# Optimization experiments

Hardware: AMD Instinct MI355X
Metric: run time of the kernel (lower is better)

## Reference

```python
import jax, jax.numpy as jnp
import numpy as np
import math

D_PAIR = 64
N_HEADS = 4
D_HEAD = D_PAIR // N_HEADS


def setup_inputs() -> dict:
    key = jax.random.key(0)
    ks = jax.random.split(key, 9)
    B, L, D = 2, 256, D_PAIR
    s = 1.0 / math.sqrt(D)
    return {
        "z": jax.random.normal(ks[0], (B, L, L, D), dtype=jnp.float32),
        "ln_scale": jnp.ones((D,), jnp.float32),
        "ln_bias": jnp.zeros((D,), jnp.float32),
        "Wq": jax.random.normal(ks[1], (D, D), jnp.float32) * s,
        "Wk": jax.random.normal(ks[2], (D, D), jnp.float32) * s,
        "Wv": jax.random.normal(ks[3], (D, D), jnp.float32) * s,
        "Wg": jax.random.normal(ks[4], (D, D), jnp.float32) * s,
        "bg": jax.random.normal(ks[5], (D,), jnp.float32) * 0.02,
        "Wo": jax.random.normal(ks[6], (D, D), jnp.float32) * s,
        "bo": jax.random.normal(ks[7], (D,), jnp.float32) * 0.02,
    }


def _layernorm(x, scale, bias, eps=1e-5):
    mu = jnp.mean(x, axis=-1, keepdims=True)
    var = jnp.var(x, axis=-1, keepdims=True)
    return (x - mu) * jax.lax.rsqrt(var + eps) * scale + bias


def reference(z, ln_scale, ln_bias, Wq, Wk, Wv, Wg, bg, Wo, bo):
    B, L, _, D = z.shape
    H, Dh = N_HEADS, D_HEAD
    zn = _layernorm(z, ln_scale, ln_bias)
    # torch Linear(no bias): x @ W.T
    Q = (zn @ Wq.T).reshape(B, L, L, H, Dh)
    K = (zn @ Wk.T).reshape(B, L, L, H, Dh)
    V = (zn @ Wv.T).reshape(B, L, L, H, Dh)
    scale = 1.0 / math.sqrt(Dh)
    # row-wise attention: for each row l, attend over column index j
    attn = jnp.einsum("blihd,bljhd->blhij", Q, K) * scale  # [B,L,H,L,L]
    attn = jax.nn.softmax(attn, axis=-1)
    out = jnp.einsum("blhij,bljhd->blihd", attn, V).reshape(B, L, L, D)
    gate = jax.nn.sigmoid(zn @ Wg.T + bg)
    out = gate * out
    return out @ Wo.T + bo
```

## Files before the change

kernel.cpp:

```cpp
#include <hip/hip_runtime.h>
#include <hip/hip_bf16.h>
#include <math.h>


typedef __attribute__((ext_vector_type(4))) float f32x4;
typedef __attribute__((ext_vector_type(8))) short s16x8;

#define MFMA16(a, b, c) __builtin_amdgcn_mfma_f32_16x16x32_bf16((a), (b), (c), 0, 0, 0)

__device__ __forceinline__ unsigned pk2(float a, float b) {
    union { __hip_bfloat162 h; unsigned u; } c;
    float2 t; t.x = a; t.y = b;
    c.h = __float22bfloat162_rn(t);
    return c.u;
}
__device__ __forceinline__ s16x8 cvt8(const float* p) {
    union { unsigned u[4]; s16x8 v; } r;
    r.u[0] = pk2(p[0], p[1]); r.u[1] = pk2(p[2], p[3]);
    r.u[2] = pk2(p[4], p[5]); r.u[3] = pk2(p[6], p[7]);
    return r.v;
}

static constexpr int ZNL = 0;
static constexpr int KSH = 16384;
static constexpr int VT  = 20480;
static constexpr int LDS_EL = 24704;

__global__ __launch_bounds__(256, 3)
void ka_fused(const float* __restrict__ z, const float* __restrict__ ln_s,
              const float* __restrict__ ln_b, const float* __restrict__ Wq,
              const float* __restrict__ Wk, const float* __restrict__ Wv,
              const float* __restrict__ Wg, const float* __restrict__ bg,
              short* __restrict__ ws)
{
    __shared__ __align__(16) short lds[LDS_EL];
    const int tid = threadIdx.x, lane = tid & 63, w = tid >> 6;
    const int n16 = lane & 15, quad = lane >> 4;
    const bool qlo = (quad < 2);
    const int g = blockIdx.x, bl = g >> 2, h = g & 3;
    const size_t rowbase = (size_t)bl * (256 * 64);
    const int wsl = w * 4096;

    {
        float zn[64];
        const float4* zp4 = (const float4*)(z + rowbase + (size_t)tid * 64);
        #pragma unroll
        for (int gq = 0; gq < 16; ++gq) {
            float4 v4 = zp4[gq];
            zn[gq * 4 + 0] = v4.x; zn[gq * 4 + 1] = v4.y;
            zn[gq * 4 + 2] = v4.z; zn[gq * 4 + 3] = v4.w;
        }
        float mu = 0.f;
        #pragma unroll
        for (int k = 0; k < 64; ++k) mu += zn[k];
        mu *= (1.f / 64.f);
        float va = 0.f;
        #pragma unroll
        for (int k = 0; k < 64; ++k) { float d = zn[k] - mu; va += d * d; }
        const float rs = rsqrtf(va * (1.f / 64.f) + 1e-5f);
        #pragma unroll
        for (int k = 0; k < 64; ++k) zn[k] = (zn[k] - mu) * rs * ln_s[k] + ln_b[k];
        const int lr = lane;
        #pragma unroll
        for (int gq = 0; gq < 8; ++gq) {
            union { unsigned u[4]; s16x8 v; } pkv;
            pkv.u[0] = pk2(zn[gq * 8 + 0], zn[gq * 8 + 1]);
            pkv.u[1] = pk2(zn[gq * 8 + 2], zn[gq * 8 + 3]);
            pkv.u[2] = pk2(zn[gq * 8 + 4], zn[gq * 8 + 5]);
            pkv.u[3] = pk2(zn[gq * 8 + 6], zn[gq * 8 + 7]);
            *(s16x8*)&lds[ZNL + wsl + (lr >> 4) * 1024 + (lr & 15) * 64
                          + ((gq ^ (lr & 7)) * 8)] = pkv.v;
        }
    }

    s16x8 bq[2], bk[2], bv[2], bgf[2];
    #pragma unroll
    for (int ks = 0; ks < 2; ++ks) {
        size_t off = (size_t)(h * 16 + n16) * 64 + ks * 32 + quad * 8;
        bq[ks] = cvt8(Wq + off);  bk[ks] = cvt8(Wk + off);
        bv[ks] = cvt8(Wv + off);  bgf[ks] = cvt8(Wg + off);
    }
    const float4 bg4 = *(const float4*)(bg + h * 16 + quad * 4);
    constexpr float QS = 0.25f * 1.44269504088896340736f;

    float g4t[4][4];
    #pragma unroll
    for (int t = 0; t < 4; ++t) {
        s16x8 zn0 = *(const s16x8*)&lds[ZNL + wsl + t * 1024 + n16 * 64
                                        + ((quad ^ (n16 & 7)) * 8)];
        s16x8 zn1 = *(const s16x8*)&lds[ZNL + wsl + t * 1024 + n16 * 64
                                        + (((4 + quad) ^ (n16 & 7)) * 8)];
        f32x4 aq = {}, ak = {}, av = {}, ag = {};
        aq = MFMA16(bq[0], zn0, aq);  aq = MFMA16(bq[1], zn1, aq);
        ak = MFMA16(bk[0], zn0, ak);  ak = MFMA16(bk[1], zn1, ak);
        ag = MFMA16(bgf[0], zn0, ag); ag = MFMA16(bgf[1], zn1, ag);
        av = MFMA16(zn0, bv[0], av);  av = MFMA16(zn1, bv[1], av);
        {
            uint2 p = {pk2(aq[0] * QS, aq[1] * QS), pk2(aq[2] * QS, aq[3] * QS)};
            *(uint2*)&lds[ZNL + wsl + t * 1024 + n16 * 16 + quad * 4] = p;
        }
        {
            uint2 p = {pk2(ak[0], ak[1]), pk2(ak[2], ak[3])};
            *(uint2*)&lds[KSH + (w * 64 + t * 16 + n16) * 16 + quad * 4] = p;
        }
        {
            uint2 p = {pk2(av[0], av[1]), pk2(av[2], av[3])};
            *(uint2*)&lds[VT + n16 * 264 + (w * 64 + t * 16 + quad * 4)] = p;
        }
        #pragma unroll
        for (int r = 0; r < 4; ++r)
            g4t[t][r] = 1.f / (1.f + __expf(-(ag[r] + bg4[r])));
    }

    s16x8 qa[4];
    #pragma unroll
    for (int qt = 0; qt < 4; ++qt) {
        s16x8 q = {};
        if (qlo) q = *(const s16x8*)&lds[ZNL + wsl + qt * 1024 + n16 * 16 + quad * 8];
        qa[qt] = q;
    }
    __syncthreads();

    float lrow[4][4];
    f32x4 o4[4];
    #pragma unroll
    for (int qt = 0; qt < 4; ++qt) {
        o4[qt] = {};
        #pragma unroll
        for (int r = 0; r < 4; ++r) lrow[qt][r] = 0.f;
    }
    const int sw = (n16 ^ (n16 >> 2)) & 3;
    for (int ch = 0; ch < 8; ++ch) {
        #pragma unroll
        for (int jtl = 0; jtl < 2; ++jtl) {
            int jt = ch * 2 + jtl;
            s16x8 kf = {};
            if (qlo) kf = *(const s16x8*)&lds[KSH + (jt * 16 + n16) * 16 + quad * 8];
            const int po = (((jtl * 2 + (quad >> 1)) ^ sw) * 8) + (quad & 1) * 4;
            #pragma unroll
            for (int qt = 0; qt < 4; ++qt) {
                f32x4 zc = {};
                f32x4 s = MFMA16(kf, qa[qt], zc);
                float e0 = exp2f(s[0]), e1 = exp2f(s[1]);
                float e2 = exp2f(s[2]), e3 = exp2f(s[3]);
                lrow[qt][0] += e0; lrow[qt][1] += e1;
                lrow[qt][2] += e2; lrow[qt][3] += e3;
                uint2 p = {pk2(e0, e1), pk2(e2, e3)};
                *(uint2*)&lds[ZNL + wsl + qt * 1024 + 256 + n16 * 40 + po] = p;
            }
        }
        s16x8 vf = *(const s16x8*)&lds[VT + n16 * 264 + ch * 32 + quad * 8];
        #pragma unroll
        for (int qt = 0; qt < 4; ++qt) {
            s16x8 pf = *(const s16x8*)&lds[ZNL + wsl + qt * 1024 + 256 + n16 * 40
                                           + ((quad ^ sw) * 8)];
            o4[qt] = MFMA16(vf, pf, o4[qt]);
        }
    }

    #pragma unroll
    for (int qt = 0; qt < 4; ++qt) {
        float l = lrow[qt][0] + lrow[qt][1] + lrow[qt][2] + lrow[qt][3];
        l += __shfl_xor(l, 16);
        l += __shfl_xor(l, 32);
        const float inv = 1.f / l;
        float g0 = g4t[qt][0] * o4[qt][0] * inv;
        float g1 = g4t[qt][1] * o4[qt][1] * inv;
        float g2 = g4t[qt][2] * o4[qt][2] * inv;
        float g3 = g4t[qt][3] * o4[qt][3] * inv;
        uint2 p = {pk2(g0, g1), pk2(g2, g3)};
        short* dst = ws + (((size_t)h * 512 + bl) * 256 + w * 64 + qt * 16 + n16) * 16
                     + quad * 4;
        *(uint2*)dst = p;
    }
}

__global__ __launch_bounds__(256, 4)
void k3_out(const short* __restrict__ ws, const float* __restrict__ Wo,
            const float* __restrict__ bo, float* __restrict__ out)
{
    const int tid = threadIdx.x, lane = tid & 63, w = tid >> 6;
    const int n16 = lane & 15, quad = lane >> 4;
    const short* GO = ws;
    const int bl = blockIdx.x >> 1, half = blockIdx.x & 1;
    const int rowloc = half * 128 + w * 32;

    s16x8 bfr[4][2];
    #pragma unroll
    for (int nt = 0; nt < 4; ++nt)
        #pragma unroll
        for (int ks = 0; ks < 2; ++ks)
            bfr[nt][ks] = cvt8(Wo + (size_t)(nt * 16 + n16) * 64 + ks * 32 + quad * 8);

    f32x4 acc[2][4] = {};
    #pragma unroll
    for (int mt = 0; mt < 2; ++mt) {
        #pragma unroll
        for (int c = 0; c < 2; ++c) {
            int hp = c * 2 + (quad >> 1);
            const short* ap = &GO[(((size_t)hp * 512 + bl) * 256 + rowloc + mt * 16 + n16) * 16
                                  + (quad & 1) * 8];
            s16x8 a = *(const s16x8*)ap;
            #pragma unroll
            for (int nt = 0; nt < 4; ++nt)
                acc[mt][nt] = MFMA16(a, bfr[nt][c], acc[mt][nt]);
        }
    }
    #pragma unroll
    for (int nt = 0; nt < 4; ++nt) {
        float bov = bo[nt * 16 + n16];
        #pragma unroll
        for (int mt = 0; mt < 2; ++mt)
            #pragma unroll
            for (int r = 0; r < 4; ++r)
                out[((size_t)bl * 256 + rowloc + mt * 16 + quad * 4 + r) * 64 + nt * 16 + n16] =
                    acc[mt][nt][r] + bov;
    }
}

extern "C" void kernel_launch(void* const* d_in, const int* in_sizes, int n_in,
                              void* d_out, int out_size, void* d_ws, size_t ws_size,
                              hipStream_t stream) {
    const float* z  = (const float*)d_in[0];
    const float* ls = (const float*)d_in[1];
    const float* lb = (const float*)d_in[2];
    const float* Wq = (const float*)d_in[3];
    const float* Wk = (const float*)d_in[4];
    const float* Wv = (const float*)d_in[5];
    const float* Wg = (const float*)d_in[6];
    const float* bg = (const float*)d_in[7];
    const float* Wo = (const float*)d_in[8];
    const float* bo = (const float*)d_in[9];
    float* out = (float*)d_out;
    short* wsp = (short*)d_ws;

    hipLaunchKernelGGL(ka_fused, dim3(2048), dim3(256), 0, stream,
                       z, ls, lb, Wq, Wk, Wv, Wg, bg, wsp);
    hipLaunchKernelGGL(k3_out, dim3(1024), dim3(256), 0, stream, wsp, Wo, bo, out);
}
```

Before: 174.5 us.

## Split LayerNorm into separate kernel and shrink attention LDS for higher occupancy

```diff
diff --git a/kernel.cpp b/kernel.cpp
--- a/kernel.cpp
+++ b/kernel.cpp
@@ -21,56 +21,69 @@
     return r.v;
 }
 
-static constexpr int ZNL = 0;
-static constexpr int KSH = 16384;
-static constexpr int VT  = 20480;
-static constexpr int LDS_EL = 24704;
-
-__global__ __launch_bounds__(256, 3)
-void ka_fused(const float* __restrict__ z, const float* __restrict__ ln_s,
-              const float* __restrict__ ln_b, const float* __restrict__ Wq,
+static constexpr size_t ZNOFF = 0;
+static constexpr size_t GOOFF = (size_t)512 * 256 * 64;
+
+__global__ __launch_bounds__(256, 2)
+void kln(const float* __restrict__ z, const float* __restrict__ ln_s,
+         const float* __restrict__ ln_b, short* __restrict__ ws)
+{
+    const int tid = threadIdx.x, bl = blockIdx.x;
+    const size_t row = (size_t)bl * 256 + tid;
+    float zn[64];
+    const float4* zp4 = (const float4*)(z + row * 64);
+    #pragma unroll
+    for (int gq = 0; gq < 16; ++gq) {
+        float4 v4 = zp4[gq];
+        zn[gq * 4 + 0] = v4.x; zn[gq * 4 + 1] = v4.y;
+        zn[gq * 4 + 2] = v4.z; zn[gq * 4 + 3] = v4.w;
+    }
+    float mu = 0.f;
+    #pragma unroll
+    for (int k = 0; k < 64; ++k) mu += zn[k];
+    mu *= (1.f / 64.f);
+    float va = 0.f;
+    #pragma unroll
+    for (int k = 0; k < 64; ++k) { float d = zn[k] - mu; va += d * d; }
+    const float rs = rsqrtf(va * (1.f / 64.f) + 1e-5f);
+    #pragma unroll
+    for (int k = 0; k < 64; ++k) zn[k] = (zn[k] - mu) * rs * ln_s[k] + ln_b[k];
+    short* dst = ws + ZNOFF + row * 64;
+    #pragma unroll
+    for (int gq = 0; gq < 8; ++gq) {
+        union { unsigned u[4]; s16x8 v; } pkv;
+        pkv.u[0] = pk2(zn[gq * 8 + 0], zn[gq * 8 + 1]);
+        pkv.u[1] = pk2(zn[gq * 8 + 2], zn[gq * 8 + 3]);
+        pkv.u[2] = pk2(zn[gq * 8 + 4], zn[gq * 8 + 5]);
+        pkv.u[3] = pk2(zn[gq * 8 + 6], zn[gq * 8 + 7]);
+        *(s16x8*)&dst[gq * 8] = pkv.v;
+    }
+}
+
+static constexpr int KSH = 0;
+static constexpr int VT  = 6144;
+static constexpr int SCR = 10368;
+static constexpr int LDS_EL = 12928;
+
+__global__ __launch_bounds__(256, 5)
+void ka_fused(const short* __restrict__ zng, const float* __restrict__ Wq,
               const float* __restrict__ Wk, const float* __restrict__ Wv,
               const float* __restrict__ Wg, const float* __restrict__ bg,
-              short* __restrict__ ws)
+              short* __restrict__ go)
 {
     __shared__ __align__(16) short lds[LDS_EL];
     const int tid = threadIdx.x, lane = tid & 63, w = tid >> 6;
     const int n16 = lane & 15, quad = lane >> 4;
     const bool qlo = (quad < 2);
     const int g = blockIdx.x, bl = g >> 2, h = g & 3;
-    const size_t rowbase = (size_t)bl * (256 * 64);
-    const int wsl = w * 4096;
-
-    {
-        float zn[64];
-        const float4* zp4 = (const float4*)(z + rowbase + (size_t)tid * 64);
-        #pragma unroll
-        for (int gq = 0; gq < 16; ++gq) {
-            float4 v4 = zp4[gq];
-            zn[gq * 4 + 0] = v4.x; zn[gq * 4 + 1] = v4.y;
-            zn[gq * 4 + 2] = v4.z; zn[gq * 4 + 3] = v4.w;
-        }
-        float mu = 0.f;
-        #pragma unroll
-        for (int k = 0; k < 64; ++k) mu += zn[k];
-        mu *= (1.f / 64.f);
-        float va = 0.f;
-        #pragma unroll
-        for (int k = 0; k < 64; ++k) { float d = zn[k] - mu; va += d * d; }
-        const float rs = rsqrtf(va * (1.f / 64.f) + 1e-5f);
-        #pragma unroll
-        for (int k = 0; k < 64; ++k) zn[k] = (zn[k] - mu) * rs * ln_s[k] + ln_b[k];
-        const int lr = lane;
-        #pragma unroll
-        for (int gq = 0; gq < 8; ++gq) {
-            union { unsigned u[4]; s16x8 v; } pkv;
-            pkv.u[0] = pk2(zn[gq * 8 + 0], zn[gq * 8 + 1]);
-            pkv.u[1] = pk2(zn[gq * 8 + 2], zn[gq * 8 + 3]);
-            pkv.u[2] = pk2(zn[gq * 8 + 4], zn[gq * 8 + 5]);
-            pkv.u[3] = pk2(zn[gq * 8 + 6], zn[gq * 8 + 7]);
-            *(s16x8*)&lds[ZNL + wsl + (lr >> 4) * 1024 + (lr & 15) * 64
-                          + ((gq ^ (lr & 7)) * 8)] = pkv.v;
-        }
+    short* scr = &lds[SCR + w * 640];
+
+    s16x8 zf[4][2];
+    const short* zb = zng + ((size_t)bl * 256 + w * 64 + n16) * 64;
+    #pragma unroll
+    for (int t = 0; t < 4; ++t) {
+        zf[t][0] = *(const s16x8*)&zb[t * 1024 + quad * 8];
+        zf[t][1] = *(const s16x8*)&zb[t * 1024 + 32 + quad * 8];
     }
 
     s16x8 bq[2], bk[2], bv[2], bgf[2];
@@ -84,24 +97,21 @@
     constexpr float QS = 0.25f * 1.44269504088896340736f;
 
     float g4t[4][4];
+    s16x8 qa[4];
     #pragma unroll
     for (int t = 0; t < 4; ++t) {
-        s16x8 zn0 = *(const s16x8*)&lds[ZNL + wsl + t * 1024 + n16 * 64
-                                        + ((quad ^ (n16 & 7)) * 8)];
-        s16x8 zn1 = *(const s16x8*)&lds[ZNL + wsl + t * 1024 + n16 * 64
-                                        + (((4 + quad) ^ (n16 & 7)) * 8)];
         f32x4 aq = {}, ak = {}, av = {}, ag = {};
-        aq = MFMA16(bq[0], zn0, aq);  aq = MFMA16(bq[1], zn1, aq);
-        ak = MFMA16(bk[0], zn0, ak);  ak = MFMA16(bk[1], zn1, ak);
-        ag = MFMA16(bgf[0], zn0, ag); ag = MFMA16(bgf[1], zn1, ag);
-        av = MFMA16(zn0, bv[0], av);  av = MFMA16(zn1, bv[1], av);
+        aq = MFMA16(bq[0],  zf[t][0], aq); aq = MFMA16(bq[1],  zf[t][1], aq);
+        ak = MFMA16(bk[0],  zf[t][0], ak); ak = MFMA16(bk[1],  zf[t][1], ak);
+        ag = MFMA16(bgf[0], zf[t][0], ag); ag = MFMA16(bgf[1], zf[t][1], ag);
+        av = MFMA16(zf[t][0], bv[0], av);  av = MFMA16(zf[t][1], bv[1], av);
         {
             uint2 p = {pk2(aq[0] * QS, aq[1] * QS), pk2(aq[2] * QS, aq[3] * QS)};
-            *(uint2*)&lds[ZNL + wsl + t * 1024 + n16 * 16 + quad * 4] = p;
+            *(uint2*)&scr[n16 * 16 + quad * 4] = p;
         }
         {
             uint2 p = {pk2(ak[0], ak[1]), pk2(ak[2], ak[3])};
-            *(uint2*)&lds[KSH + (w * 64 + t * 16 + n16) * 16 + quad * 4] = p;
+            *(uint2*)&lds[KSH + (w * 64 + t * 16 + n16) * 24 + quad * 4] = p;
         }
         {
             uint2 p = {pk2(av[0], av[1]), pk2(av[2], av[3])};
@@ -110,14 +120,9 @@
         #pragma unroll
         for (int r = 0; r < 4; ++r)
             g4t[t][r] = 1.f / (1.f + __expf(-(ag[r] + bg4[r])));
-    }
-
-    s16x8 qa[4];
-    #pragma unroll
-    for (int qt = 0; qt < 4; ++qt) {
         s16x8 q = {};
-        if (qlo) q = *(const s16x8*)&lds[ZNL + wsl + qt * 1024 + n16 * 16 + quad * 8];
-        qa[qt] = q;
+        if (qlo) q = *(const s16x8*)&scr[n16 * 16 + quad * 8];
+        qa[t] = q;
     }
     __syncthreads();
 
@@ -129,31 +134,31 @@
         #pragma unroll
         for (int r = 0; r < 4; ++r) lrow[qt][r] = 0.f;
     }
-    const int sw = (n16 ^ (n16 >> 2)) & 3;
     for (int ch = 0; ch < 8; ++ch) {
-        #pragma unroll
-        for (int jtl = 0; jtl < 2; ++jtl) {
-            int jt = ch * 2 + jtl;
-            s16x8 kf = {};
-            if (qlo) kf = *(const s16x8*)&lds[KSH + (jt * 16 + n16) * 16 + quad * 8];
-            const int po = (((jtl * 2 + (quad >> 1)) ^ sw) * 8) + (quad & 1) * 4;
-            #pragma unroll
-            for (int qt = 0; qt < 4; ++qt) {
-                f32x4 zc = {};
-                f32x4 s = MFMA16(kf, qa[qt], zc);
-                float e0 = exp2f(s[0]), e1 = exp2f(s[1]);
-                float e2 = exp2f(s[2]), e3 = exp2f(s[3]);
-                lrow[qt][0] += e0; lrow[qt][1] += e1;
-                lrow[qt][2] += e2; lrow[qt][3] += e3;
-                uint2 p = {pk2(e0, e1), pk2(e2, e3)};
-                *(uint2*)&lds[ZNL + wsl + qt * 1024 + 256 + n16 * 40 + po] = p;
-            }
+        s16x8 kf0 = {}, kf1 = {};
+        if (qlo) {
+            kf0 = *(const s16x8*)&lds[KSH + ((ch * 2 + 0) * 16 + n16) * 24 + quad * 8];
+            kf1 = *(const s16x8*)&lds[KSH + ((ch * 2 + 1) * 16 + n16) * 24 + quad * 8];
         }
         s16x8 vf = *(const s16x8*)&lds[VT + n16 * 264 + ch * 32 + quad * 8];
         #pragma unroll
         for (int qt = 0; qt < 4; ++qt) {
-            s16x8 pf = *(const s16x8*)&lds[ZNL + wsl + qt * 1024 + 256 + n16 * 40
-                                           + ((quad ^ sw) * 8)];
+            f32x4 zc = {};
+            f32x4 s0 = MFMA16(kf0, qa[qt], zc);
+            float e0 = exp2f(s0[0]), e1 = exp2f(s0[1]);
+            float e2 = exp2f(s0[2]), e3 = exp2f(s0[3]);
+            lrow[qt][0] += e0; lrow[qt][1] += e1;
+            lrow[qt][2] += e2; lrow[qt][3] += e3;
+            uint2 p0 = {pk2(e0, e1), pk2(e2, e3)};
+            *(uint2*)&scr[n16 * 40 + quad * 4] = p0;
+            f32x4 s1 = MFMA16(kf1, qa[qt], zc);
+            float f0 = exp2f(s1[0]), f1 = exp2f(s1[1]);
+            float f2 = exp2f(s1[2]), f3 = exp2f(s1[3]);
+            lrow[qt][0] += f0; lrow[qt][1] += f1;
+            lrow[qt][2] += f2; lrow[qt][3] += f3;
+            uint2 p1 = {pk2(f0, f1), pk2(f2, f3)};
+            *(uint2*)&scr[n16 * 40 + 16 + quad * 4] = p1;
+            s16x8 pf = *(const s16x8*)&scr[n16 * 40 + quad * 8];
             o4[qt] = MFMA16(vf, pf, o4[qt]);
         }
     }
@@ -169,19 +174,18 @@
         float g2 = g4t[qt][2] * o4[qt][2] * inv;
         float g3 = g4t[qt][3] * o4[qt][3] * inv;
         uint2 p = {pk2(g0, g1), pk2(g2, g3)};
-        short* dst = ws + (((size_t)h * 512 + bl) * 256 + w * 64 + qt * 16 + n16) * 16
+        short* dst = go + (((size_t)h * 512 + bl) * 256 + w * 64 + qt * 16 + n16) * 16
                      + quad * 4;
         *(uint2*)dst = p;
     }
 }
 
 __global__ __launch_bounds__(256, 4)
-void k3_out(const short* __restrict__ ws, const float* __restrict__ Wo,
+void k3_out(const short* __restrict__ go, const float* __restrict__ Wo,
             const float* __restrict__ bo, float* __restrict__ out)
 {
     const int tid = threadIdx.x, lane = tid & 63, w = tid >> 6;
     const int n16 = lane & 15, quad = lane >> 4;
-    const short* GO = ws;
     const int bl = blockIdx.x >> 1, half = blockIdx.x & 1;
     const int rowloc = half * 128 + w * 32;
 
@@ -198,7 +202,7 @@
         #pragma unroll
         for (int c = 0; c < 2; ++c) {
             int hp = c * 2 + (quad >> 1);
-            const short* ap = &GO[(((size_t)hp * 512 + bl) * 256 + rowloc + mt * 16 + n16) * 16
+            const short* ap = &go[(((size_t)hp * 512 + bl) * 256 + rowloc + mt * 16 + n16) * 16
                                   + (quad & 1) * 8];
             s16x8 a = *(const s16x8*)ap;
             #pragma unroll
@@ -234,7 +238,8 @@
     float* out = (float*)d_out;
     short* wsp = (short*)d_ws;
 
+    hipLaunchKernelGGL(kln, dim3(512), dim3(256), 0, stream, z, ls, lb, wsp + ZNOFF);
     hipLaunchKernelGGL(ka_fused, dim3(2048), dim3(256), 0, stream,
-                       z, ls, lb, Wq, Wk, Wv, Wg, bg, wsp);
-    hipLaunchKernelGGL(k3_out, dim3(1024), dim3(256), 0, stream, wsp, Wo, bo, out);
-}
+                       wsp + ZNOFF, Wq, Wk, Wv, Wg, bg, wsp + GOOFF);
+    hipLaunchKernelGGL(k3_out, dim3(1024), dim3(256), 0, stream, wsp + GOOFF, Wo, bo, out);
+}
```

Result: slower. 375.3 us (+115.0%).
